# Kernel tuning notes

Measured on AMD Instinct MI355X. Metric: run time of the kernel, lower is better.

The kernel has to match this reference:

```python
import jax, jax.numpy as jnp
import numpy as np

RADIUS = 8
NUM = 200
EPS = 1e-8


def _conv2d(x, k, pad_mode):
    # x: [B,1,H,W], k: [kh,kw]; same-size conv with given numpy-style padding mode
    ph, pw = k.shape[0] // 2, k.shape[1] // 2
    xp = jnp.pad(x, ((0, 0), (0, 0), (ph, ph), (pw, pw)), mode=pad_mode)
    return jax.lax.conv_general_dilated(
        xp, k[None, None], (1, 1), 'VALID',
        dimension_numbers=('NCHW', 'OIHW', 'NCHW'))


def _gauss_kernel7():
    xs = np.arange(7, dtype=np.float32) - 3.0
    g = np.exp(-0.5 * xs ** 2)
    g /= g.sum()
    return jnp.asarray(np.outer(g, g))


def get_corners(imgs):
    B, _, H, W = imgs.shape
    # kornia rgb_to_grayscale
    gray = 0.299 * imgs[:, 0:1] + 0.587 * imgs[:, 1:2] + 0.114 * imgs[:, 2:3]
    # kornia CornerGFTT: sobel gradients (normalized), gaussian-smoothed structure tensor, min eigenvalue
    sob = jnp.array([[-1., 0., 1.], [-2., 0., 2.], [-1., 0., 1.]], jnp.float32) / 8.0
    dx = _conv2d(gray, sob, 'edge')
    dy = _conv2d(gray, sob.T, 'edge')
    g = _gauss_kernel7()
    dx2 = _conv2d(dx * dx, g, 'reflect')
    dy2 = _conv2d(dy * dy, g, 'reflect')
    dxy = _conv2d(dx * dy, g, 'reflect')
    tr = dx2 + dy2
    det = dx2 * dy2 - dxy * dxy
    resp = 0.5 * (tr - jnp.sqrt(jnp.abs(tr * tr - 4.0 * det)))  # GFTT score (min eigval)
    # kornia nms2d with 5x5 window: keep local maxima
    mp = jax.lax.reduce_window(resp, -jnp.inf, jax.lax.max,
                               (1, 1, 5, 5), (1, 1, 1, 1),
                               [(0, 0), (0, 0), (2, 2), (2, 2)])
    resp = jnp.where(resp == mp, resp, 0.0)
    # unfold/mask/fold with kernel=stride=RADIUS == per non-overlapping 8x8 block:
    # keep elements equal to the block max and > 0
    r = RADIUS
    blk = resp.reshape(B, 1, H // r, r, W // r, r)
    bmax = blk.max(axis=(3, 5), keepdims=True)
    blk = jnp.where((blk > 0) & (blk == bmax), blk, 0.0)
    corners = blk.reshape(B, H * W)
    # top-200 scatter then binarize
    vals, idx = jax.lax.top_k(corners, NUM)
    out = jnp.zeros_like(corners).at[jnp.arange(B)[:, None], idx].set(vals)
    return (out > 0).astype(imgs.dtype).reshape(B, 1, H, W)


def setup_inputs() -> dict:
    key = jax.random.key(0)
    k1, k2, k3, k4 = jax.random.split(key, 4)
    B, N, D, H, W = 16, 2048, 256, 384, 384
    return {
        'descriptors': jax.random.normal(k1, (B, N, D), jnp.float32),
        'scores': jax.random.uniform(k2, (B, N), jnp.float32),
        'scores_dense': jax.random.normal(k3, (B, 1, H, W), jnp.float32),
        'imgs': jax.random.uniform(k4, (B, 3, H, W), jnp.float32),
    }


def reference(descriptors, scores, scores_dense, imgs):
    corners = get_corners(imgs)
    # all-pairs cosine similarity within each batch: pcos[b,i,j]
    norms = jnp.linalg.norm(descriptors, axis=-1)  # [B,N]
    dots = jnp.einsum('bnd,bmd->bnm', descriptors, descriptors)
    pcos = dots / jnp.maximum(norms[:, :, None] * norms[:, None, :], EPS)
    # BCEWithLogitsLoss(scores_dense, corners), mean reduction
    bce = jnp.mean(jnp.logaddexp(0.0, scores_dense) - scores_dense * corners)
    return bce + jnp.mean(jax.nn.relu(pcos))
```

## Files before the change

kernel.cpp:

```cpp
#include <hip/hip_runtime.h>

#define H 384
#define W 384
#define HWSZ (H * W)
#define NB 16
#define ND 2048
#define DD 256

#define OFF_RESP  256
#define OFF_CVAL  9437440
#define OFF_CPOS  9584896
#define OFF_DESCB 9732352
#define OFF_INV   26509568
#define OFF_PSOFT 26640640
#define OFF_PGEMM 26643200
#define OFF_PCORN 26652160

__device__ __forceinline__ int clampi(int v) { return v < 0 ? 0 : (v > 383 ? 383 : v); }
__device__ __forceinline__ int refl(int v) { return v < 0 ? -v : (v >= 384 ? 766 - v : v); }

__device__ __forceinline__ unsigned f2e4m3(float x) {
  float a = fabsf(x);
  unsigned s = (__float_as_uint(x) >> 31) << 7;
  if (a >= 448.f) return s | 0x7E;
  if (a < 0.015625f) {
    int m = (int)rintf(a * 512.f);
    return s | (unsigned)m;
  }
  unsigned u = __float_as_uint(a);
  u += 0x7FFFF + ((u >> 20) & 1);
  unsigned e = (u >> 23) - 120;
  unsigned m = (u >> 20) & 7;
  return s | (e << 3) | m;
}

typedef float f32x4 __attribute__((ext_vector_type(4)));

__device__ __forceinline__ void load_lds16(const void* g, void* l) {
  __builtin_amdgcn_global_load_lds((const __attribute__((address_space(1))) void*)g,
                                   (__attribute__((address_space(3))) void*)l, 16, 0, 0);
}

__global__ __launch_bounds__(256) void stage1_kernel(const float* __restrict__ imgs,
                                                     float* __restrict__ resp,
                                                     const float* __restrict__ desc,
                                                     unsigned char* __restrict__ descF8,
                                                     float* __restrict__ invn) {
  __shared__ float pbuf[4448];
  __shared__ float ubuf[3648];
  float* p0 = pbuf;
  float* p1 = pbuf + 1482;
  float* p2 = pbuf + 2964;
  float* glf = ubuf;
  float* t0 = ubuf;
  float* t1 = ubuf + 1216;
  float* t2 = ubuf + 2432;

  if (blockIdx.x >= 2304) {
    int wave = threadIdx.x >> 6, lane = threadIdx.x & 63;
    int row = (blockIdx.x - 2304) * 4 + wave;
    const float4* src = (const float4*)(desc + (size_t)row * DD);
    float4 v = src[lane];
    unsigned pk = f2e4m3(v.x) | (f2e4m3(v.y) << 8) | (f2e4m3(v.z) << 16) | (f2e4m3(v.w) << 24);
    ((unsigned*)(descF8 + (size_t)row * DD))[lane] = pk;
    float ss = v.x * v.x + v.y * v.y + v.z * v.z + v.w * v.w;
    for (int off = 32; off; off >>= 1) ss += __shfl_down(ss, off, 64);
    if (lane == 0) invn[row] = 1.f / fmaxf(sqrtf(ss), 1e-4f);
    return;
  }

  const float GW[7] = {0.0044330482f, 0.0540055826f, 0.2420362294f, 0.3990502160f,
                       0.2420362294f, 0.0540055826f, 0.0044330482f};
  int bid = blockIdx.x;
  int b = bid / 144;
  int t = bid % 144;
  int Y0 = (t / 12) * 32, X0 = (t % 12) * 32;
  const float* ib = imgs + (size_t)b * 3 * HWSZ;

  for (int i = threadIdx.x; i < 1600; i += 256) {
    int r = i / 40, c = i % 40;
    int gy = clampi(Y0 - 4 + r), gx = clampi(X0 - 4 + c);
    const float* p = ib + gy * W + gx;
    glf[r * 41 + c] = 0.299f * p[0] + 0.587f * p[HWSZ] + 0.114f * p[2 * HWSZ];
  }
  __syncthreads();

  bool interior = (X0 >= 32 && X0 <= 320 && Y0 >= 32 && Y0 <= 320);

  if (interior) {
    for (int i = threadIdx.x; i < 1444; i += 256) {
      int r = i / 38, c = i % 38;
      const float* g0 = glf + r * 41 + c;
      float a = g0[0],  bb = g0[1],  cc = g0[2];
      float d = g0[41],              e = g0[43];
      float f = g0[82], g = g0[83],  h = g0[84];
      float dx = 0.125f * ((cc - a) + 2.f * (e - d) + (h - f));
      float dy = 0.125f * ((f - a) + 2.f * (g - bb) + (h - cc));
      p0[r * 39 + c] = dx * dx;
      p1[r * 39 + c] = dy * dy;
      p2[r * 39 + c] = dx * dy;
    }
  } else {
    for (int i = threadIdx.x; i < 1444; i += 256) {
      int r = i / 38, c = i % 38;
      int py = refl(Y0 - 3 + r), px = refl(X0 - 3 + c);
      int ym = clampi(py - 1) - (Y0 - 4), y0 = py - (Y0 - 4), yp = clampi(py + 1) - (Y0 - 4);
      int xm = clampi(px - 1) - (X0 - 4), x0 = px - (X0 - 4), xp = clampi(px + 1) - (X0 - 4);
      float a = glf[ym * 41 + xm], bb = glf[ym * 41 + x0], cc = glf[ym * 41 + xp];
      float d = glf[y0 * 41 + xm], e = glf[y0 * 41 + xp];
      float f = glf[yp * 41 + xm], g = glf[yp * 41 + x0], h = glf[yp * 41 + xp];
      float dx = 0.125f * ((cc - a) + 2.f * (e - d) + (h - f));
      float dy = 0.125f * ((f - a) + 2.f * (g - bb) + (h - cc));
      p0[r * 39 + c] = dx * dx;
      p1[r * 39 + c] = dy * dy;
      p2[r * 39 + c] = dx * dy;
    }
  }
  __syncthreads();

  for (int g = threadIdx.x; g < 304; g += 256) {
    int r = g >> 3, c0 = (g & 7) * 4;
    {
      float a[10];
#pragma unroll
      for (int dc = 0; dc < 10; dc++) a[dc] = p0[r * 39 + c0 + dc];
#pragma unroll
      for (int k = 0; k < 4; k++) {
        float sv = 0.f;
#pragma unroll
        for (int j = 0; j < 7; j++) sv += GW[j] * a[k + j];
        t0[r * 32 + c0 + k] = sv;
      }
    }
    {
      float a[10];
#pragma unroll
      for (int dc = 0; dc < 10; dc++) a[dc] = p1[r * 39 + c0 + dc];
#pragma unroll
      for (int k = 0; k < 4; k++) {
        float sv = 0.f;
#pragma unroll
        for (int j = 0; j < 7; j++) sv += GW[j] * a[k + j];
        t1[r * 32 + c0 + k] = sv;
      }
    }
    {
      float a[10];
#pragma unroll
      for (int dc = 0; dc < 10; dc++) a[dc] = p2[r * 39 + c0 + dc];
#pragma unroll
      for (int k = 0; k < 4; k++) {
        float sv = 0.f;
#pragma unroll
        for (int j = 0; j < 7; j++) sv += GW[j] * a[k + j];
        t2[r * 32 + c0 + k] = sv;
      }
    }
  }
  __syncthreads();

  {
    int r0 = (threadIdx.x >> 5) * 4, c = threadIdx.x & 31;
    float s0[4], s1[4], s2[4];
    {
      float a[10];
#pragma unroll
      for (int dr = 0; dr < 10; dr++) a[dr] = t0[(r0 + dr) * 32 + c];
#pragma unroll
      for (int k = 0; k < 4; k++) {
        float sv = 0.f;
#pragma unroll
        for (int j = 0; j < 7; j++) sv += GW[j] * a[k + j];
        s0[k] = sv;
      }
    }
    {
      float a[10];
#pragma unroll
      for (int dr = 0; dr < 10; dr++) a[dr] = t1[(r0 + dr) * 32 + c];
#pragma unroll
      for (int k = 0; k < 4; k++) {
        float sv = 0.f;
#pragma unroll
        for (int j = 0; j < 7; j++) sv += GW[j] * a[k + j];
        s1[k] = sv;
      }
    }
    {
      float a[10];
#pragma unroll
      for (int dr = 0; dr < 10; dr++) a[dr] = t2[(r0 + dr) * 32 + c];
#pragma unroll
      for (int k = 0; k < 4; k++) {
        float sv = 0.f;
#pragma unroll
        for (int j = 0; j < 7; j++) sv += GW[j] * a[k + j];
        s2[k] = sv;
      }
    }
#pragma unroll
    for (int k = 0; k < 4; k++) {
      float tr = s0[k] + s1[k];
      float det = s0[k] * s1[k] - s2[k] * s2[k];
      float disc = tr * tr - 4.f * det;
      float rv = 0.5f * (tr - sqrtf(fabsf(disc)));
      resp[(size_t)b * HWSZ + (Y0 + r0 + k) * W + (X0 + c)] = rv;
    }
  }
}

__global__ __launch_bounds__(256) void stage2_kernel(const float* __restrict__ resp,
                                                     float* __restrict__ cval,
                                                     unsigned* __restrict__ cpos,
                                                     const float4* __restrict__ sd4,
                                                     float* __restrict__ psoft) {
  __shared__ float rl[68][69];
  __shared__ float nl[64][65];
  __shared__ float r4[4];

  if (blockIdx.x >= 576) {
    int sb = blockIdx.x - 576;
    float s = 0.f;
    int base = sb * 256 + threadIdx.x;
#pragma unroll
    for (int it = 0; it < 4; it++) {
      float4 v = sd4[base + it * 147456];
      s += fmaxf(v.x, 0.f) + log1pf(expf(-fabsf(v.x))) +
           fmaxf(v.y, 0.f) + log1pf(expf(-fabsf(v.y))) +
           fmaxf(v.z, 0.f) + log1pf(expf(-fabsf(v.z))) +
           fmaxf(v.w, 0.f) + log1pf(expf(-fabsf(v.w)));
    }
    for (int off = 32; off; off >>= 1) s += __shfl_down(s, off, 64);
    if ((threadIdx.x & 63) == 0) r4[threadIdx.x >> 6] = s;
    __syncthreads();
    if (threadIdx.x == 0) psoft[sb] = r4[0] + r4[1] + r4[2] + r4[3];
    return;
  }

  int bid = blockIdx.x;
  int b = bid / 36;
  int t = bid % 36;
  int Y0 = (t / 6) * 64, X0 = (t % 6) * 64;
  const float* rb = resp + (size_t)b * HWSZ;

  for (int i = threadIdx.x; i < 68 * 68; i += 256) {
    int r = i / 68, c = i % 68;
    int gy = Y0 - 2 + r, gx = X0 - 2 + c;
    float v = -INFINITY;
    if (gy >= 0 && gy < H && gx >= 0 && gx < W) v = rb[gy * W + gx];
    rl[r][c] = v;
  }
  __syncthreads();

  for (int i = threadIdx.x; i < 4096; i += 256) {
    int r = i / 64, c = i % 64;
    float m = -INFINITY;
#pragma unroll
    for (int dr = 0; dr < 5; dr++)
#pragma unroll
      for (int dc = 0; dc < 5; dc++) m = fmaxf(m, rl[r + dr][c + dc]);
    float v = rl[r + 2][c + 2];
    nl[r][c] = (v == m) ? v : 0.f;
  }
  __syncthreads();

  if (threadIdx.x < 64) {
    int bi = threadIdx.x / 8, bj = threadIdx.x % 8;
    float bv = 0.f;
    unsigned bp = 0;
    for (int rr = 0; rr < 8; rr++)
      for (int cc = 0; cc < 8; cc++) {
        float v = nl[bi * 8 + rr][bj * 8 + cc];
        if (v > bv) { bv = v; bp = (unsigned)((Y0 + bi * 8 + rr) * W + (X0 + bj * 8 + cc)); }
      }
    int ci = b * 2304 + (Y0 / 8 + bi) * 48 + (X0 / 8 + bj);
    cval[ci] = bv;
    cpos[ci] = bp;
  }
}

__global__ __launch_bounds__(256) void stage3_kernel(const float* __restrict__ cval,
                                                     const unsigned* __restrict__ cpos,
                                                     const float* __restrict__ sd,
                                                     float* __restrict__ pcorn,
                                                     const unsigned char* __restrict__ descF8,
                                                     const float* __restrict__ invn,
                                                     float* __restrict__ pgemm) {
  __shared__ char lA[128 * 128];
  __shared__ char lB[128 * 128];
  __shared__ float r4[4];
  __shared__ int hist[256];
  __shared__ int pick[2];
  __shared__ unsigned eqpos[256];
  __shared__ int eqcnt;
  __shared__ int ri[4];

  if (blockIdx.x < 16) {
    int b = blockIdx.x;
    int t = threadIdx.x;
    int lane = t & 63;

    unsigned bits[9], pos[9];
#pragma unroll
    for (int q = 0; q < 9; q++) {
      int i = t + q * 256;
      unsigned vb = 0, p = 0;
      if (i < 2304) {
        float v = cval[b * 2304 + i];
        if (v > 0.f) { vb = __float_as_uint(v); p = cpos[b * 2304 + i]; }
      }
      bits[q] = vb; pos[q] = p;
    }

    int P = 0;
#pragma unroll
    for (int q = 0; q < 9; q++) P += (bits[q] != 0u);
    for (int off = 32; off; off >>= 1) P += __shfl_down(P, off, 64);
    if (lane == 0) ri[t >> 6] = P;
    __syncthreads();
    int Ptot = ri[0] + ri[1] + ri[2] + ri[3];
    if (Ptot == 0) { if (t == 0) pcorn[b] = 0.f; return; }
    int K = Ptot < 200 ? Ptot : 200;

    unsigned prefix = 0;
    int krem = K;
    for (int shift = 24; shift >= 0; shift -= 8) {
      hist[t] = 0;
      __syncthreads();
#pragma unroll
      for (int q = 0; q < 9; q++) {
        if (bits[q] != 0u &&
            (shift == 24 || (bits[q] >> (shift + 8)) == (prefix >> (shift + 8))))
          atomicAdd(&hist[(bits[q] >> shift) & 0xFF], 1);
      }
      __syncthreads();
      if (t < 64) {
        int h0 = hist[4 * t], h1 = hist[4 * t + 1], h2 = hist[4 * t + 2], h3 = hist[4 * t + 3];
        int tot = h0 + h1 + h2 + h3;
        int acc = tot;
        for (int d = 1; d < 64; d <<= 1) {
          int o = __shfl_down(acc, d, 64);
          if (t + d < 64) acc += o;
        }
        int excl = acc - tot;
        int G3 = excl, G2 = excl + h3, G1 = excl + h3 + h2, G0 = excl + h3 + h2 + h1;
        if (G0 < krem && G0 + h0 >= krem) { pick[0] = 4 * t;     pick[1] = G0; }
        if (G1 < krem && G1 + h1 >= krem) { pick[0] = 4 * t + 1; pick[1] = G1; }
        if (G2 < krem && G2 + h2 >= krem) { pick[0] = 4 * t + 2; pick[1] = G2; }
        if (G3 < krem && G3 + h3 >= krem) { pick[0] = 4 * t + 3; pick[1] = G3; }
      }
      __syncthreads();
      prefix |= ((unsigned)pick[0]) << shift;
      krem -= pick[1];
      __syncthreads();
    }

    if (t == 0) eqcnt = 0;
    __syncthreads();
    float s = 0.f;
#pragma unroll
    for (int q = 0; q < 9; q++) {
      if (bits[q] > prefix) s += sd[(size_t)b * HWSZ + pos[q]];
      else if (bits[q] != 0u && bits[q] == prefix) {
        int idx = atomicAdd(&eqcnt, 1);
        if (idx < 256) eqpos[idx] = pos[q];
      }
    }
    __syncthreads();
    int m = eqcnt;
    if (m <= krem) {
      if (t < m) s += sd[(size_t)b * HWSZ + eqpos[t]];
    } else {
      int mm = m < 256 ? m : 256;
      if (t < mm) {
        unsigned p = eqpos[t];
        int rank = 0;
        for (int u = 0; u < mm; u++) rank += (eqpos[u] < p);
        if (rank < krem) s += sd[(size_t)b * HWSZ + p];
      }
    }
    for (int off = 32; off; off >>= 1) s += __shfl_down(s, off, 64);
    if (lane == 0) r4[t >> 6] = s;
    __syncthreads();
    if (t == 0) pcorn[b] = r4[0] + r4[1] + r4[2] + r4[3];
    return;
  }

  int bx = blockIdx.x - 16;
  int batch = bx / 136;
  int rem = bx % 136;
  int ti = 0, rowlen = 16;
  while (rem >= rowlen) { rem -= rowlen; rowlen--; ti++; }
  int tj = ti + rem;

  const unsigned char* Ab = descF8 + (size_t)batch * ND * DD;
  const float* inv = invn + batch * ND;
  int I0 = ti * 128, J0 = tj * 128;

  int tid = threadIdx.x;
  int wave = tid >> 6, lane = tid & 63;
  int rm = lane & 15, kq = lane >> 4;
  int wr = wave >> 1, wc = wave & 1;
  int lrow = lane >> 3;
  int lcolb = ((lane & 7) ^ lrow) << 4;
  int cx = rm & 7;

  f32x4 accf[4][4];
#pragma unroll
  for (int m = 0; m < 4; m++)
#pragma unroll
    for (int n = 0; n < 4; n++) accf[m][n] = (f32x4){0.f, 0.f, 0.f, 0.f};

  for (int k0 = 0; k0 < DD; k0 += 128) {
#pragma unroll
    for (int q = 0; q < 4; q++) {
      int chunk = wave * 4 + q;
      load_lds16(Ab + (size_t)(I0 + chunk * 8 + lrow) * DD + k0 + lcolb, lA + chunk * 1024);
      load_lds16(Ab + (size_t)(J0 + chunk * 8 + lrow) * DD + k0 + lcolb, lB + chunk * 1024);
    }
    __syncthreads();
#pragma unroll
    for (int kk = 0; kk < 128; kk += 32) {
      long af[4], bfr[4];
      int koff = kk + kq * 8;
      int pcol = ((((koff >> 4) ^ cx) << 4) | (koff & 8));
#pragma unroll
      for (int m = 0; m < 4; m++)
        af[m] = *reinterpret_cast<const long*>(lA + (wr * 64 + m * 16 + rm) * 128 + pcol);
#pragma unroll
      for (int n = 0; n < 4; n++)
        bfr[n] = *reinterpret_cast<const long*>(lB + (wc * 64 + n * 16 + rm) * 128 + pcol);
#pragma unroll
      for (int m = 0; m < 4; m++)
#pragma unroll
        for (int n = 0; n < 4; n++)
          accf[m][n] = __builtin_amdgcn_mfma_f32_16x16x32_fp8_fp8(af[m], bfr[n], accf[m][n], 0, 0, 0);
    }
    __syncthreads();
  }

  float wgt = (ti == tj) ? 1.f : 2.f;
  float invC[4];
#pragma unroll
  for (int n = 0; n < 4; n++) invC[n] = inv[J0 + wc * 64 + n * 16 + rm];
  float psum = 0.f;
#pragma unroll
  for (int m = 0; m < 4; m++) {
#pragma unroll
    for (int r = 0; r < 4; r++) {
      float invR = inv[I0 + wr * 64 + m * 16 + kq * 4 + r];
#pragma unroll
      for (int n = 0; n < 4; n++) psum += fmaxf(accf[m][n][r] * invR * invC[n], 0.f);
    }
  }
  psum *= wgt;
  for (int off = 32; off; off >>= 1) psum += __shfl_down(psum, off, 64);
  if (lane == 0) r4[wave] = psum;
  __syncthreads();
  if (tid == 0) pgemm[bx] = r4[0] + r4[1] + r4[2] + r4[3];
}

__global__ __launch_bounds__(256) void finalize_kernel(const float* __restrict__ psoft,
                                                       const float* __restrict__ pcorn,
                                                       const float* __restrict__ pgemm,
                                                       float* __restrict__ out) {
  __shared__ float r4[4];
  float bce = 0.f;
  for (int i = threadIdx.x; i < 576; i += 256) bce += psoft[i];
  if (threadIdx.x < 16) bce -= pcorn[threadIdx.x];
  float g = 0.f;
  for (int i = threadIdx.x; i < 2176; i += 256) g += pgemm[i];
  float t = bce * (1.f / 2359296.f) + g * (1.f / 67108864.f);
  for (int off = 32; off; off >>= 1) t += __shfl_down(t, off, 64);
  if ((threadIdx.x & 63) == 0) r4[threadIdx.x >> 6] = t;
  __syncthreads();
  if (threadIdx.x == 0) out[0] = r4[0] + r4[1] + r4[2] + r4[3];
}

extern "C" void kernel_launch(void* const* d_in, const int* in_sizes, int n_in,
                              void* d_out, int out_size, void* d_ws, size_t ws_size,
                              hipStream_t stream) {
  (void)in_sizes; (void)n_in; (void)out_size; (void)ws_size;
  const float* desc = (const float*)d_in[0];
  const float* sd = (const float*)d_in[2];
  const float* imgs = (const float*)d_in[3];
  float* out = (float*)d_out;

  char* w = (char*)d_ws;
  float* resp = (float*)(w + OFF_RESP);
  float* cval = (float*)(w + OFF_CVAL);
  unsigned* cpos = (unsigned*)(w + OFF_CPOS);
  unsigned char* descF8 = (unsigned char*)(w + OFF_DESCB);
  float* invn = (float*)(w + OFF_INV);
  float* psoft = (float*)(w + OFF_PSOFT);
  float* pgemm = (float*)(w + OFF_PGEMM);
  float* pcorn = (float*)(w + OFF_PCORN);

  stage1_kernel<<<10496, 256, 0, stream>>>(imgs, resp, desc, descF8, invn);
  stage2_kernel<<<1152, 256, 0, stream>>>(resp, cval, cpos, (const float4*)sd, psoft);
  stage3_kernel<<<2192, 256, 0, stream>>>(cval, cpos, sd, pcorn, descF8, invn, pgemm);
  finalize_kernel<<<1, 256, 0, stream>>>(psoft, pcorn, pgemm, out);
}
```

Baseline: 158.5 us.

## Move cosine GEMM into stage2 and fold finalize into top-k kernel

Moves the FP8 MFMA all-pairs cosine GEMM blocks from stage3 into the stage2 launch, where they run next to the NMS and softplus blocks and share one smem buffer. The GEMM tiles are remapped with a stride so consecutive blocks touch different batches. The separate finalize kernel is dropped: the 16 top-k blocks now use an atomic counter, and the last block to finish does the final reduction. This saves a launch and lets the GEMM overlap the memory-bound stage2 work. In exchange it adds atomics and raises LDS use per block, which can lower occupancy for the lighter block types.

```diff
diff --git a/kernel.cpp b/kernel.cpp
--- a/kernel.cpp
+++ b/kernel.cpp
@@ -15,6 +15,7 @@
 #define OFF_PSOFT 26640640
 #define OFF_PGEMM 26643200
 #define OFF_PCORN 26652160
+#define OFF_CNT   26652224
 
 __device__ __forceinline__ int clampi(int v) { return v < 0 ? 0 : (v > 383 ? 383 : v); }
 __device__ __forceinline__ int refl(int v) { return v < 0 ? -v : (v >= 384 ? 766 - v : v); }
@@ -213,13 +214,98 @@
                                                      float* __restrict__ cval,
                                                      unsigned* __restrict__ cpos,
                                                      const float4* __restrict__ sd4,
-                                                     float* __restrict__ psoft) {
-  __shared__ float rl[68][69];
-  __shared__ float nl[64][65];
-  __shared__ float r4[4];
-
-  if (blockIdx.x >= 576) {
-    int sb = blockIdx.x - 576;
+                                                     float* __restrict__ psoft,
+                                                     const unsigned char* __restrict__ descF8,
+                                                     const float* __restrict__ invn,
+                                                     float* __restrict__ pgemm,
+                                                     int* __restrict__ cnt3) {
+  alignas(16) __shared__ char smem[35408];
+
+  if (blockIdx.x < 2176) {
+    char* lA = smem;
+    char* lB = smem + 16384;
+    float* r4 = (float*)(smem + 32768);
+
+    int bx = blockIdx.x;
+    bx = ((bx & 7) * 272) + (bx >> 3);
+    int batch = bx / 136;
+    int rem = bx % 136;
+    int ti = 0, rowlen = 16;
+    while (rem >= rowlen) { rem -= rowlen; rowlen--; ti++; }
+    int tj = ti + rem;
+
+    const unsigned char* Ab = descF8 + (size_t)batch * ND * DD;
+    const float* inv = invn + batch * ND;
+    int I0 = ti * 128, J0 = tj * 128;
+
+    int tid = threadIdx.x;
+    int wave = tid >> 6, lane = tid & 63;
+    int rm = lane & 15, kq = lane >> 4;
+    int wr = wave >> 1, wc = wave & 1;
+    int lrow = lane >> 3;
+    int lcolb = ((lane & 7) ^ lrow) << 4;
+    int cx = rm & 7;
+
+    f32x4 accf[4][4];
+#pragma unroll
+    for (int m = 0; m < 4; m++)
+#pragma unroll
+      for (int n = 0; n < 4; n++) accf[m][n] = (f32x4){0.f, 0.f, 0.f, 0.f};
+
+    for (int k0 = 0; k0 < DD; k0 += 128) {
+#pragma unroll
+      for (int q = 0; q < 4; q++) {
+        int chunk = wave * 4 + q;
+        load_lds16(Ab + (size_t)(I0 + chunk * 8 + lrow) * DD + k0 + lcolb, lA + chunk * 1024);
+        load_lds16(Ab + (size_t)(J0 + chunk * 8 + lrow) * DD + k0 + lcolb, lB + chunk * 1024);
+      }
+      __syncthreads();
+#pragma unroll
+      for (int kk = 0; kk < 128; kk += 32) {
+        long af[4], bfr[4];
+        int koff = kk + kq * 8;
+        int pcol = ((((koff >> 4) ^ cx) << 4) | (koff & 8));
+#pragma unroll
+        for (int m = 0; m < 4; m++)
+          af[m] = *reinterpret_cast<const long*>(lA + (wr * 64 + m * 16 + rm) * 128 + pcol);
+#pragma unroll
+        for (int n = 0; n < 4; n++)
+          bfr[n] = *reinterpret_cast<const long*>(lB + (wc * 64 + n * 16 + rm) * 128 + pcol);
+#pragma unroll
+        for (int m = 0; m < 4; m++)
+#pragma unroll
+          for (int n = 0; n < 4; n++)
+            accf[m][n] = __builtin_amdgcn_mfma_f32_16x16x32_fp8_fp8(af[m], bfr[n], accf[m][n], 0, 0, 0);
+      }
+      __syncthreads();
+    }
+
+    float wgt = (ti == tj) ? 1.f : 2.f;
+    float invC[4];
+#pragma unroll
+    for (int n = 0; n < 4; n++) invC[n] = inv[J0 + wc * 64 + n * 16 + rm];
+    float psum = 0.f;
+#pragma unroll
+    for (int m = 0; m < 4; m++) {
+#pragma unroll
+      for (int r = 0; r < 4; r++) {
+        float invR = inv[I0 + wr * 64 + m * 16 + kq * 4 + r];
+#pragma unroll
+        for (int n = 0; n < 4; n++) psum += fmaxf(accf[m][n][r] * invR * invC[n], 0.f);
+      }
+    }
+    psum *= wgt;
+    for (int off = 32; off; off >>= 1) psum += __shfl_down(psum, off, 64);
+    if (lane == 0) r4[wave] = psum;
+    __syncthreads();
+    if (tid == 0) pgemm[bx] = r4[0] + r4[1] + r4[2] + r4[3];
+    return;
+  }
+
+  if (blockIdx.x >= 2752) {
+    int sb = blockIdx.x - 2752;
+    float* r4 = (float*)smem;
+    if (sb == 0 && threadIdx.x == 0) *cnt3 = 0;
     float s = 0.f;
     int base = sb * 256 + threadIdx.x;
 #pragma unroll
@@ -237,7 +323,10 @@
     return;
   }
 
-  int bid = blockIdx.x;
+  float (*rl)[69] = (float (*)[69])smem;
+  float (*nl)[65] = (float (*)[65])(smem + 18768);
+
+  int bid = blockIdx.x - 2176;
   int b = bid / 36;
   int t = bid % 36;
   int Y0 = (t / 6) * 64, X0 = (t % 6) * 64;
@@ -283,43 +372,44 @@
                                                      const unsigned* __restrict__ cpos,
                                                      const float* __restrict__ sd,
                                                      float* __restrict__ pcorn,
-                                                     const unsigned char* __restrict__ descF8,
-                                                     const float* __restrict__ invn,
-                                                     float* __restrict__ pgemm) {
-  __shared__ char lA[128 * 128];
-  __shared__ char lB[128 * 128];
-  __shared__ float r4[4];
+                                                     const float* __restrict__ psoft,
+                                                     const float* __restrict__ pgemm,
+                                                     int* __restrict__ cnt3,
+                                                     float* __restrict__ out) {
   __shared__ int hist[256];
   __shared__ int pick[2];
   __shared__ unsigned eqpos[256];
   __shared__ int eqcnt;
   __shared__ int ri[4];
-
-  if (blockIdx.x < 16) {
-    int b = blockIdx.x;
-    int t = threadIdx.x;
-    int lane = t & 63;
-
-    unsigned bits[9], pos[9];
-#pragma unroll
-    for (int q = 0; q < 9; q++) {
-      int i = t + q * 256;
-      unsigned vb = 0, p = 0;
-      if (i < 2304) {
-        float v = cval[b * 2304 + i];
-        if (v > 0.f) { vb = __float_as_uint(v); p = cpos[b * 2304 + i]; }
-      }
-      bits[q] = vb; pos[q] = p;
-    }
-
-    int P = 0;
-#pragma unroll
-    for (int q = 0; q < 9; q++) P += (bits[q] != 0u);
-    for (int off = 32; off; off >>= 1) P += __shfl_down(P, off, 64);
-    if (lane == 0) ri[t >> 6] = P;
-    __syncthreads();
-    int Ptot = ri[0] + ri[1] + ri[2] + ri[3];
-    if (Ptot == 0) { if (t == 0) pcorn[b] = 0.f; return; }
+  __shared__ float r4[4];
+  __shared__ int lastFlag;
+
+  int b = blockIdx.x;
+  int t = threadIdx.x;
+  int lane = t & 63;
+
+  unsigned bits[9], pos[9];
+#pragma unroll
+  for (int q = 0; q < 9; q++) {
+    int i = t + q * 256;
+    unsigned vb = 0, p = 0;
+    if (i < 2304) {
+      float v = cval[b * 2304 + i];
+      if (v > 0.f) { vb = __float_as_uint(v); p = cpos[b * 2304 + i]; }
+    }
+    bits[q] = vb; pos[q] = p;
+  }
+
+  int P = 0;
+#pragma unroll
+  for (int q = 0; q < 9; q++) P += (bits[q] != 0u);
+  for (int off = 32; off; off >>= 1) P += __shfl_down(P, off, 64);
+  if (lane == 0) ri[t >> 6] = P;
+  __syncthreads();
+  int Ptot = ri[0] + ri[1] + ri[2] + ri[3];
+
+  float total = 0.f;
+  if (Ptot > 0) {
     int K = Ptot < 200 ? Ptot : 200;
 
     unsigned prefix = 0;
@@ -382,99 +472,27 @@
     for (int off = 32; off; off >>= 1) s += __shfl_down(s, off, 64);
     if (lane == 0) r4[t >> 6] = s;
     __syncthreads();
-    if (t == 0) pcorn[b] = r4[0] + r4[1] + r4[2] + r4[3];
-    return;
-  }
-
-  int bx = blockIdx.x - 16;
-  int batch = bx / 136;
-  int rem = bx % 136;
-  int ti = 0, rowlen = 16;
-  while (rem >= rowlen) { rem -= rowlen; rowlen--; ti++; }
-  int tj = ti + rem;
-
-  const unsigned char* Ab = descF8 + (size_t)batch * ND * DD;
-  const float* inv = invn + batch * ND;
-  int I0 = ti * 128, J0 = tj * 128;
-
-  int tid = threadIdx.x;
-  int wave = tid >> 6, lane = tid & 63;
-  int rm = lane & 15, kq = lane >> 4;
-  int wr = wave >> 1, wc = wave & 1;
-  int lrow = lane >> 3;
-  int lcolb = ((lane & 7) ^ lrow) << 4;
-  int cx = rm & 7;
-
-  f32x4 accf[4][4];
-#pragma unroll
-  for (int m = 0; m < 4; m++)
-#pragma unroll
-    for (int n = 0; n < 4; n++) accf[m][n] = (f32x4){0.f, 0.f, 0.f, 0.f};
-
-  for (int k0 = 0; k0 < DD; k0 += 128) {
-#pragma unroll
-    for (int q = 0; q < 4; q++) {
-      int chunk = wave * 4 + q;
-      load_lds16(Ab + (size_t)(I0 + chunk * 8 + lrow) * DD + k0 + lcolb, lA + chunk * 1024);
-      load_lds16(Ab + (size_t)(J0 + chunk * 8 + lrow) * DD + k0 + lcolb, lB + chunk * 1024);
-    }
-    __syncthreads();
-#pragma unroll
-    for (int kk = 0; kk < 128; kk += 32) {
-      long af[4], bfr[4];
-      int koff = kk + kq * 8;
-      int pcol = ((((koff >> 4) ^ cx) << 4) | (koff & 8));
-#pragma unroll
-      for (int m = 0; m < 4; m++)
-        af[m] = *reinterpret_cast<const long*>(lA + (wr * 64 + m * 16 + rm) * 128 + pcol);
-#pragma unroll
-      for (int n = 0; n < 4; n++)
-        bfr[n] = *reinterpret_cast<const long*>(lB + (wc * 64 + n * 16 + rm) * 128 + pcol);
-#pragma unroll
-      for (int m = 0; m < 4; m++)
-#pragma unroll
-        for (int n = 0; n < 4; n++)
-          accf[m][n] = __builtin_amdgcn_mfma_f32_16x16x32_fp8_fp8(af[m], bfr[n], accf[m][n], 0, 0, 0);
-    }
-    __syncthreads();
-  }
-
-  float wgt = (ti == tj) ? 1.f : 2.f;
-  float invC[4];
-#pragma unroll
-  for (int n = 0; n < 4; n++) invC[n] = inv[J0 + wc * 64 + n * 16 + rm];
-  float psum = 0.f;
-#pragma unroll
-  for (int m = 0; m < 4; m++) {
-#pragma unroll
-    for (int r = 0; r < 4; r++) {
-      float invR = inv[I0 + wr * 64 + m * 16 + kq * 4 + r];
-#pragma unroll
-      for (int n = 0; n < 4; n++) psum += fmaxf(accf[m][n][r] * invR * invC[n], 0.f);
-    }
-  }
-  psum *= wgt;
-  for (int off = 32; off; off >>= 1) psum += __shfl_down(psum, off, 64);
-  if (lane == 0) r4[wave] = psum;
-  __syncthreads();
-  if (tid == 0) pgemm[bx] = r4[0] + r4[1] + r4[2] + r4[3];
-}
-
-__global__ __launch_bounds__(256) void finalize_kernel(const float* __restrict__ psoft,
-                                                       const float* __restrict__ pcorn,
-                                                       const float* __restrict__ pgemm,
-                                                       float* __restrict__ out) {
-  __shared__ float r4[4];
+    total = r4[0] + r4[1] + r4[2] + r4[3];
+  }
+
+  if (t == 0) {
+    atomicExch(&pcorn[b], total);
+    __threadfence();
+    lastFlag = (atomicAdd(cnt3, 1) == 15);
+  }
+  __syncthreads();
+  if (!lastFlag) return;
+
   float bce = 0.f;
-  for (int i = threadIdx.x; i < 576; i += 256) bce += psoft[i];
-  if (threadIdx.x < 16) bce -= pcorn[threadIdx.x];
+  for (int i = t; i < 576; i += 256) bce += psoft[i];
+  if (t < 16) bce -= atomicAdd(&pcorn[t], 0.f);
   float g = 0.f;
-  for (int i = threadIdx.x; i < 2176; i += 256) g += pgemm[i];
-  float t = bce * (1.f / 2359296.f) + g * (1.f / 67108864.f);
-  for (int off = 32; off; off >>= 1) t += __shfl_down(t, off, 64);
-  if ((threadIdx.x & 63) == 0) r4[threadIdx.x >> 6] = t;
-  __syncthreads();
-  if (threadIdx.x == 0) out[0] = r4[0] + r4[1] + r4[2] + r4[3];
+  for (int i = t; i < 2176; i += 256) g += pgemm[i];
+  float v = bce * (1.f / 2359296.f) + g * (1.f / 67108864.f);
+  for (int off = 32; off; off >>= 1) v += __shfl_down(v, off, 64);
+  if (lane == 0) r4[t >> 6] = v;
+  __syncthreads();
+  if (t == 0) out[0] = r4[0] + r4[1] + r4[2] + r4[3];
 }
 
 extern "C" void kernel_launch(void* const* d_in, const int* in_sizes, int n_in,
@@ -495,9 +513,10 @@
   float* psoft = (float*)(w + OFF_PSOFT);
   float* pgemm = (float*)(w + OFF_PGEMM);
   float* pcorn = (float*)(w + OFF_PCORN);
+  int* cnt3 = (int*)(w + OFF_CNT);
 
   stage1_kernel<<<10496, 256, 0, stream>>>(imgs, resp, desc, descF8, invn);
-  stage2_kernel<<<1152, 256, 0, stream>>>(resp, cval, cpos, (const float4*)sd, psoft);
-  stage3_kernel<<<2192, 256, 0, stream>>>(cval, cpos, sd, pcorn, descF8, invn, pgemm);
-  finalize_kernel<<<1, 256, 0, stream>>>(psoft, pcorn, pgemm, out);
+  stage2_kernel<<<3328, 256, 0, stream>>>(resp, cval, cpos, (const float4*)sd, psoft,
+                                          descF8, invn, pgemm, cnt3);
+  stage3_kernel<<<16, 256, 0, stream>>>(cval, cpos, sd, pcorn, psoft, pgemm, cnt3, out);
 }
```

Measured after the change: 168.5 us. 1.06x slower.
